# Optimization experiments

Hardware: AMD Instinct MI355X
Metric: run time of the kernel (lower is better)

The kernel has to match this reference:

```python
import jax, jax.numpy as jnp
import numpy as np


def setup_inputs() -> dict:
    key = jax.random.key(0)
    kA, kW = jax.random.split(key, 2)
    T, N = 64, 128  # seq_len, num_peds
    A = jax.random.normal(kA, (T, N, N), dtype=jnp.float32)
    # Linear(2N -> 1): weight stored as (2N, 1), bias (1,)
    W = jax.random.normal(kW, (2 * N, 1), dtype=jnp.float32) * (1.0 / np.sqrt(2 * N))
    b = jnp.zeros((1,), dtype=jnp.float32)
    return {"A": A, "W": W, "b": b}


def reference(A, W, b):
    # A: (T, N, N). Original loops over timesteps; here fully vectorized.
    N = A.shape[2]
    aT = jnp.swapaxes(A, 1, 2)            # a_ = a_.T per timestep -> (T, N, N)
    # Pairwise concat [aT[i], aT[j]] fed to Linear(2N->1) decomposes exactly:
    # score[t,i,j] = aT[t,i]@w1 + aT[t,j]@w2 + b
    w1, w2 = W[:N, 0], W[N:, 0]           # (N,), (N,)
    s1 = aT @ w1                           # (T, N) row-i contribution
    s2 = aT @ w2                           # (T, N) row-j contribution
    e = jax.nn.leaky_relu(s1[:, :, None] + s2[:, None, :] + b[0],
                          negative_slope=0.2)   # (T, N, N)
    alpha = jax.nn.softmax(e, axis=2)      # softmax over neighbor index j (torch dim=1 of (N,N,1))
    # GAT-style aggregation: out[t,i,f] = sum_j alpha[t,i,j] * aT[t,j,f]
    return jnp.einsum('tij,tjf->tif', alpha, aT)
```

## Files before the change

kernel.cpp:

```cpp
#include <hip/hip_runtime.h>

#define NN 128

typedef __attribute__((ext_vector_type(8))) short short8;
typedef __attribute__((ext_vector_type(4))) float f32x4;

__device__ __forceinline__ int SWZ(int r, int cs) {
    return (r << 7) + (cs ^ ((r & 7) << 3));
}

__device__ __forceinline__ unsigned asu(float x) { return __float_as_uint(x); }
__device__ __forceinline__ float asf(unsigned u) { return __uint_as_float(u); }

__global__ __launch_bounds__(256, 2) void gat_fused(
    const float* __restrict__ A, const float* __restrict__ W,
    const float* __restrict__ b, float* __restrict__ out)
{
    __shared__ unsigned short Ah_s[NN * NN];
    __shared__ unsigned short Al_s[NN * NN];
    __shared__ float w_s[2 * NN];
    __shared__ float part1_s[4 * NN], part2_s[4 * NN];
    __shared__ float s1_s[NN], s2_s[NN];

    const int tid  = threadIdx.x;
    const int lane = tid & 63;
    const int wid  = tid >> 6;
    const int t    = blockIdx.x & 63;
    const int i0   = (blockIdx.x >> 6) << 4;
    const float* At = A + (size_t)t * NN * NN;
    const float b0 = b[0];

    if (tid < 64)
        reinterpret_cast<float4*>(w_s)[tid] = reinterpret_cast<const float4*>(W)[tid];
    __syncthreads();

    {
        const float4* A4 = reinterpret_cast<const float4*>(At);
        float p1[4] = {0,0,0,0}, p2[4] = {0,0,0,0};
        #pragma unroll
        for (int it = 0; it < 16; ++it) {
            int e4 = it * 256 + tid;
            int f  = e4 >> 5;
            int cs = (e4 & 31) << 2;
            float4 v = A4[e4];
            float wf1 = w_s[f], wf2 = w_s[NN + f];
            p1[0] += wf1 * v.x; p1[1] += wf1 * v.y; p1[2] += wf1 * v.z; p1[3] += wf1 * v.w;
            p2[0] += wf2 * v.x; p2[1] += wf2 * v.y; p2[2] += wf2 * v.z; p2[3] += wf2 * v.w;
            unsigned ux = asu(v.x), uy = asu(v.y), uz = asu(v.z), uw = asu(v.w);
            float rx = v.x - asf(ux & 0xffff0000u);
            float ry = v.y - asf(uy & 0xffff0000u);
            float rz = v.z - asf(uz & 0xffff0000u);
            float rw = v.w - asf(uw & 0xffff0000u);
            uint2 hv, lv;
            hv.x = (ux >> 16) | (uy & 0xffff0000u);
            hv.y = (uz >> 16) | (uw & 0xffff0000u);
            lv.x = (asu(rx) >> 16) | (asu(ry) & 0xffff0000u);
            lv.y = (asu(rz) >> 16) | (asu(rw) & 0xffff0000u);
            int idx = SWZ(f, cs);
            *reinterpret_cast<uint2*>(&Ah_s[idx]) = hv;
            *reinterpret_cast<uint2*>(&Al_s[idx]) = lv;
        }
        #pragma unroll
        for (int q = 0; q < 4; ++q) {
            p1[q] += __shfl_xor(p1[q], 32);
            p2[q] += __shfl_xor(p2[q], 32);
        }
        if (lane < 32) {
            float4 v1 = { p1[0], p1[1], p1[2], p1[3] };
            float4 v2 = { p2[0], p2[1], p2[2], p2[3] };
            *reinterpret_cast<float4*>(&part1_s[wid * NN + lane * 4]) = v1;
            *reinterpret_cast<float4*>(&part2_s[wid * NN + lane * 4]) = v2;
        }
    }
    __syncthreads();

    if (tid < NN) {
        s1_s[tid] = part1_s[tid] + part1_s[NN + tid]
                  + part1_s[2 * NN + tid] + part1_s[3 * NN + tid] + b0;
        s2_s[tid] = part2_s[tid] + part2_s[NN + tid]
                  + part2_s[2 * NN + tid] + part2_s[3 * NN + tid];
    }
    __syncthreads();

    {
        const int f0 = wid * 32;
        const int ar = lane & 15;
        const int kg = (lane >> 4) << 3;

        short8 bh0[4], bh1[4], bl0[4], bl1[4];
        #pragma unroll
        for (int k = 0; k < 4; ++k) {
            int c = k * 32 + kg;
            bh0[k] = *reinterpret_cast<const short8*>(&Ah_s[SWZ(f0 + ar, c)]);
            bh1[k] = *reinterpret_cast<const short8*>(&Ah_s[SWZ(f0 + 16 + ar, c)]);
            bl0[k] = *reinterpret_cast<const short8*>(&Al_s[SWZ(f0 + ar, c)]);
            bl1[k] = *reinterpret_cast<const short8*>(&Al_s[SWZ(f0 + 16 + ar, c)]);
        }

        float s1v = s1_s[i0 + ar];
        float ev[32];
        float m = -3.4e38f;
        #pragma unroll
        for (int k = 0; k < 4; ++k) {
            float4 sa = *reinterpret_cast<const float4*>(&s2_s[k * 32 + kg]);
            float4 sb = *reinterpret_cast<const float4*>(&s2_s[k * 32 + kg + 4]);
            float xs[8] = { sa.x, sa.y, sa.z, sa.w, sb.x, sb.y, sb.z, sb.w };
            #pragma unroll
            for (int e = 0; e < 8; ++e) {
                float x = s1v + xs[e];
                x = (x >= 0.f) ? x : 0.2f * x;
                ev[k * 8 + e] = x;
                m = fmaxf(m, x);
            }
        }
        m = fmaxf(m, __shfl_xor(m, 16));
        m = fmaxf(m, __shfl_xor(m, 32));
        float s = 0.f;
        #pragma unroll
        for (int c = 0; c < 32; ++c) { ev[c] = __expf(ev[c] - m); s += ev[c]; }
        s += __shfl_xor(s, 16);
        s += __shfl_xor(s, 32);
        float inv = 1.0f / s;

        short8 ah[4], al[4];
        #pragma unroll
        for (int k = 0; k < 4; ++k) {
            union { short8 s8; uint4 u4; } H, L;
            #pragma unroll
            for (int p = 0; p < 4; ++p) {
                float v0 = ev[k * 8 + 2 * p]     * inv;
                float v1 = ev[k * 8 + 2 * p + 1] * inv;
                unsigned u0 = asu(v0), u1 = asu(v1);
                float r0 = v0 - asf(u0 & 0xffff0000u);
                float r1 = v1 - asf(u1 & 0xffff0000u);
                unsigned hw = (u0 >> 16) | (u1 & 0xffff0000u);
                unsigned lw = (asu(r0) >> 16) | (asu(r1) & 0xffff0000u);
                if (p == 0) { H.u4.x = hw; L.u4.x = lw; }
                else if (p == 1) { H.u4.y = hw; L.u4.y = lw; }
                else if (p == 2) { H.u4.z = hw; L.u4.z = lw; }
                else { H.u4.w = hw; L.u4.w = lw; }
            }
            ah[k] = H.s8;
            al[k] = L.s8;
        }

        f32x4 acc0 = {0.f,0.f,0.f,0.f}, acc1 = {0.f,0.f,0.f,0.f};
        #pragma unroll
        for (int k = 0; k < 4; ++k) {
            acc0 = __builtin_amdgcn_mfma_f32_16x16x32_bf16(ah[k], bh0[k], acc0, 0, 0, 0);
            acc1 = __builtin_amdgcn_mfma_f32_16x16x32_bf16(ah[k], bh1[k], acc1, 0, 0, 0);
        }
        #pragma unroll
        for (int k = 0; k < 4; ++k) {
            acc0 = __builtin_amdgcn_mfma_f32_16x16x32_bf16(ah[k], bl0[k], acc0, 0, 0, 0);
            acc1 = __builtin_amdgcn_mfma_f32_16x16x32_bf16(ah[k], bl1[k], acc1, 0, 0, 0);
        }
        #pragma unroll
        for (int k = 0; k < 4; ++k) {
            acc0 = __builtin_amdgcn_mfma_f32_16x16x32_bf16(al[k], bh0[k], acc0, 0, 0, 0);
            acc1 = __builtin_amdgcn_mfma_f32_16x16x32_bf16(al[k], bh1[k], acc1, 0, 0, 0);
        }

        float* outt = out + (size_t)t * NN * NN;
        int orow = i0 + ((lane >> 4) << 2);
        int col  = lane & 15;
        #pragma unroll
        for (int q = 0; q < 4; ++q) {
            outt[(orow + q) * NN + f0 + col]      = acc0[q];
            outt[(orow + q) * NN + f0 + 16 + col] = acc1[q];
        }
    }
}

extern "C" void kernel_launch(void* const* d_in, const int* in_sizes, int n_in,
                              void* d_out, int out_size, void* d_ws, size_t ws_size,
                              hipStream_t stream) {
    const float* A = (const float*)d_in[0];
    const float* W = (const float*)d_in[1];
    const float* b = (const float*)d_in[2];
    float* out = (float*)d_out;
    gat_fused<<<dim3(512), dim3(256), 0, stream>>>(A, W, b, out);
}
```

Measured before the change: 11.64 us.

## Split score computation into separate kernel and drop shared-memory A staging

Replaces the single fused kernel, in which each of 512 blocks recomputed s1/s2 over the whole 128x128 timestep slice and staged it in LDS as bf16 hi/lo, with two kernels. The first computes s1/s2 once per timestep into workspace. The second launches 1024 LDS-free blocks, each loading its own B fragment straight from global memory and splitting it into bf16 hi/lo in registers, with one 16x16 output tile per wave. This removes redundant score computation and the LDS traffic, at the cost of an extra launch, a dependency through global workspace, and B fragments being loaded again by many blocks.

```diff
diff --git a/kernel.cpp b/kernel.cpp
--- a/kernel.cpp
+++ b/kernel.cpp
@@ -5,171 +5,148 @@
 typedef __attribute__((ext_vector_type(8))) short short8;
 typedef __attribute__((ext_vector_type(4))) float f32x4;
 
-__device__ __forceinline__ int SWZ(int r, int cs) {
-    return (r << 7) + (cs ^ ((r & 7) << 3));
-}
-
 __device__ __forceinline__ unsigned asu(float x) { return __float_as_uint(x); }
 __device__ __forceinline__ float asf(unsigned u) { return __uint_as_float(u); }
 
-__global__ __launch_bounds__(256, 2) void gat_fused(
+__device__ __forceinline__ void hilo2(float v0, float v1, unsigned& hw, unsigned& lw) {
+    unsigned u0 = asu(v0), u1 = asu(v1);
+    float r0 = v0 - asf(u0 & 0xffff0000u);
+    float r1 = v1 - asf(u1 & 0xffff0000u);
+    hw = (u0 >> 16) | (u1 & 0xffff0000u);
+    lw = (asu(r0) >> 16) | (asu(r1) & 0xffff0000u);
+}
+
+__global__ __launch_bounds__(256) void s_compute(
     const float* __restrict__ A, const float* __restrict__ W,
-    const float* __restrict__ b, float* __restrict__ out)
+    const float* __restrict__ b, float* __restrict__ s_ws)
 {
-    __shared__ unsigned short Ah_s[NN * NN];
-    __shared__ unsigned short Al_s[NN * NN];
     __shared__ float w_s[2 * NN];
     __shared__ float part1_s[4 * NN], part2_s[4 * NN];
-    __shared__ float s1_s[NN], s2_s[NN];
-
-    const int tid  = threadIdx.x;
-    const int lane = tid & 63;
-    const int wid  = tid >> 6;
-    const int t    = blockIdx.x & 63;
-    const int i0   = (blockIdx.x >> 6) << 4;
+    const int tid = threadIdx.x, lane = tid & 63, wid = tid >> 6;
+    const int t = blockIdx.x;
     const float* At = A + (size_t)t * NN * NN;
-    const float b0 = b[0];
 
     if (tid < 64)
         reinterpret_cast<float4*>(w_s)[tid] = reinterpret_cast<const float4*>(W)[tid];
     __syncthreads();
 
-    {
-        const float4* A4 = reinterpret_cast<const float4*>(At);
-        float p1[4] = {0,0,0,0}, p2[4] = {0,0,0,0};
+    const float4* A4 = reinterpret_cast<const float4*>(At);
+    float p1[4] = {0,0,0,0}, p2[4] = {0,0,0,0};
+    #pragma unroll
+    for (int it = 0; it < 16; ++it) {
+        int e4 = it * 256 + tid;
+        int f  = e4 >> 5;
+        float4 v = A4[e4];
+        float w1 = w_s[f], w2 = w_s[NN + f];
+        p1[0] += w1 * v.x; p1[1] += w1 * v.y; p1[2] += w1 * v.z; p1[3] += w1 * v.w;
+        p2[0] += w2 * v.x; p2[1] += w2 * v.y; p2[2] += w2 * v.z; p2[3] += w2 * v.w;
+    }
+    #pragma unroll
+    for (int q = 0; q < 4; ++q) {
+        p1[q] += __shfl_xor(p1[q], 32);
+        p2[q] += __shfl_xor(p2[q], 32);
+    }
+    if (lane < 32) {
+        float4 v1 = { p1[0], p1[1], p1[2], p1[3] };
+        float4 v2 = { p2[0], p2[1], p2[2], p2[3] };
+        *reinterpret_cast<float4*>(&part1_s[wid * NN + lane * 4]) = v1;
+        *reinterpret_cast<float4*>(&part2_s[wid * NN + lane * 4]) = v2;
+    }
+    __syncthreads();
+    if (tid < NN) {
+        s_ws[t * NN + tid] = part1_s[tid] + part1_s[NN + tid]
+                           + part1_s[2 * NN + tid] + part1_s[3 * NN + tid] + b[0];
+    } else {
+        int c = tid - NN;
+        s_ws[64 * NN + t * NN + c] = part2_s[c] + part2_s[NN + c]
+                                   + part2_s[2 * NN + c] + part2_s[3 * NN + c];
+    }
+}
+
+__global__ __launch_bounds__(256, 4) void gat_pv(
+    const float* __restrict__ A, const float* __restrict__ s_ws,
+    float* __restrict__ out)
+{
+    const int tid  = threadIdx.x;
+    const int lane = tid & 63, wid = tid >> 6;
+    const int bid  = blockIdx.x;
+    const int t    = bid & 63;
+    const int f0   = ((bid >> 6) & 7) << 4;
+    const int i0   = ((bid >> 9) << 6) + (wid << 4);
+    const int r    = lane & 15;
+    const int g    = lane >> 4;
+
+    const float* Brow = A + (size_t)t * NN * NN + (size_t)(f0 + r) * NN + g * 8;
+    float4 bv[8];
+    #pragma unroll
+    for (int k = 0; k < 4; ++k) {
+        bv[2 * k]     = *reinterpret_cast<const float4*>(Brow + 32 * k);
+        bv[2 * k + 1] = *reinterpret_cast<const float4*>(Brow + 32 * k + 4);
+    }
+    const float* s2p = s_ws + 64 * NN + t * NN + g * 8;
+    float4 s2v[8];
+    #pragma unroll
+    for (int k = 0; k < 4; ++k) {
+        s2v[2 * k]     = *reinterpret_cast<const float4*>(s2p + 32 * k);
+        s2v[2 * k + 1] = *reinterpret_cast<const float4*>(s2p + 32 * k + 4);
+    }
+    float s1v = s_ws[t * NN + i0 + r];
+
+    float ev[32];
+    float m = -3.4e38f;
+    #pragma unroll
+    for (int q = 0; q < 8; ++q) {
+        float xs[4] = { s2v[q].x, s2v[q].y, s2v[q].z, s2v[q].w };
         #pragma unroll
-        for (int it = 0; it < 16; ++it) {
-            int e4 = it * 256 + tid;
-            int f  = e4 >> 5;
-            int cs = (e4 & 31) << 2;
-            float4 v = A4[e4];
-            float wf1 = w_s[f], wf2 = w_s[NN + f];
-            p1[0] += wf1 * v.x; p1[1] += wf1 * v.y; p1[2] += wf1 * v.z; p1[3] += wf1 * v.w;
-            p2[0] += wf2 * v.x; p2[1] += wf2 * v.y; p2[2] += wf2 * v.z; p2[3] += wf2 * v.w;
-            unsigned ux = asu(v.x), uy = asu(v.y), uz = asu(v.z), uw = asu(v.w);
-            float rx = v.x - asf(ux & 0xffff0000u);
-            float ry = v.y - asf(uy & 0xffff0000u);
-            float rz = v.z - asf(uz & 0xffff0000u);
-            float rw = v.w - asf(uw & 0xffff0000u);
-            uint2 hv, lv;
-            hv.x = (ux >> 16) | (uy & 0xffff0000u);
-            hv.y = (uz >> 16) | (uw & 0xffff0000u);
-            lv.x = (asu(rx) >> 16) | (asu(ry) & 0xffff0000u);
-            lv.y = (asu(rz) >> 16) | (asu(rw) & 0xffff0000u);
-            int idx = SWZ(f, cs);
-            *reinterpret_cast<uint2*>(&Ah_s[idx]) = hv;
-            *reinterpret_cast<uint2*>(&Al_s[idx]) = lv;
-        }
-        #pragma unroll
-        for (int q = 0; q < 4; ++q) {
-            p1[q] += __shfl_xor(p1[q], 32);
-            p2[q] += __shfl_xor(p2[q], 32);
-        }
-        if (lane < 32) {
-            float4 v1 = { p1[0], p1[1], p1[2], p1[3] };
-            float4 v2 = { p2[0], p2[1], p2[2], p2[3] };
-            *reinterpret_cast<float4*>(&part1_s[wid * NN + lane * 4]) = v1;
-            *reinterpret_cast<float4*>(&part2_s[wid * NN + lane * 4]) = v2;
+        for (int e = 0; e < 4; ++e) {
+            float x = s1v + xs[e];
+            x = (x >= 0.f) ? x : 0.2f * x;
+            ev[q * 4 + e] = x;
+            m = fmaxf(m, x);
         }
     }
-    __syncthreads();
+    m = fmaxf(m, __shfl_xor(m, 16));
+    m = fmaxf(m, __shfl_xor(m, 32));
+    float s = 0.f;
+    #pragma unroll
+    for (int c = 0; c < 32; ++c) { ev[c] = __expf(ev[c] - m); s += ev[c]; }
+    s += __shfl_xor(s, 16);
+    s += __shfl_xor(s, 32);
+    const float inv = 1.0f / s;
 
-    if (tid < NN) {
-        s1_s[tid] = part1_s[tid] + part1_s[NN + tid]
-                  + part1_s[2 * NN + tid] + part1_s[3 * NN + tid] + b0;
-        s2_s[tid] = part2_s[tid] + part2_s[NN + tid]
-                  + part2_s[2 * NN + tid] + part2_s[3 * NN + tid];
+    short8 ah[4], al[4], bh[4], bl[4];
+    #pragma unroll
+    for (int k = 0; k < 4; ++k) {
+        union { short8 s8; unsigned u[4]; } H, L;
+        #pragma unroll
+        for (int p = 0; p < 4; ++p)
+            hilo2(ev[8 * k + 2 * p] * inv, ev[8 * k + 2 * p + 1] * inv, H.u[p], L.u[p]);
+        ah[k] = H.s8; al[k] = L.s8;
     }
-    __syncthreads();
+    #pragma unroll
+    for (int k = 0; k < 4; ++k) {
+        union { short8 s8; unsigned u[4]; } H, L;
+        hilo2(bv[2 * k].x,     bv[2 * k].y,     H.u[0], L.u[0]);
+        hilo2(bv[2 * k].z,     bv[2 * k].w,     H.u[1], L.u[1]);
+        hilo2(bv[2 * k + 1].x, bv[2 * k + 1].y, H.u[2], L.u[2]);
+        hilo2(bv[2 * k + 1].z, bv[2 * k + 1].w, H.u[3], L.u[3]);
+        bh[k] = H.s8; bl[k] = L.s8;
+    }
 
-    {
-        const int f0 = wid * 32;
-        const int ar = lane & 15;
-        const int kg = (lane >> 4) << 3;
+    f32x4 acc = {0.f, 0.f, 0.f, 0.f};
+    #pragma unroll
+    for (int k = 0; k < 4; ++k)
+        acc = __builtin_amdgcn_mfma_f32_16x16x32_bf16(ah[k], bh[k], acc, 0, 0, 0);
+    #pragma unroll
+    for (int k = 0; k < 4; ++k)
+        acc = __builtin_amdgcn_mfma_f32_16x16x32_bf16(ah[k], bl[k], acc, 0, 0, 0);
+    #pragma unroll
+    for (int k = 0; k < 4; ++k)
+        acc = __builtin_amdgcn_mfma_f32_16x16x32_bf16(al[k], bh[k], acc, 0, 0, 0);
 
-        short8 bh0[4], bh1[4], bl0[4], bl1[4];
-        #pragma unroll
-        for (int k = 0; k < 4; ++k) {
-            int c = k * 32 + kg;
-            bh0[k] = *reinterpret_cast<const short8*>(&Ah_s[SWZ(f0 + ar, c)]);
-            bh1[k] = *reinterpret_cast<const short8*>(&Ah_s[SWZ(f0 + 16 + ar, c)]);
-            bl0[k] = *reinterpret_cast<const short8*>(&Al_s[SWZ(f0 + ar, c)]);
-            bl1[k] = *reinterpret_cast<const short8*>(&Al_s[SWZ(f0 + 16 + ar, c)]);
-        }
-
-        float s1v = s1_s[i0 + ar];
-        float ev[32];
-        float m = -3.4e38f;
-        #pragma unroll
-        for (int k = 0; k < 4; ++k) {
-            float4 sa = *reinterpret_cast<const float4*>(&s2_s[k * 32 + kg]);
-            float4 sb = *reinterpret_cast<const float4*>(&s2_s[k * 32 + kg + 4]);
-            float xs[8] = { sa.x, sa.y, sa.z, sa.w, sb.x, sb.y, sb.z, sb.w };
-            #pragma unroll
-            for (int e = 0; e < 8; ++e) {
-                float x = s1v + xs[e];
-                x = (x >= 0.f) ? x : 0.2f * x;
-                ev[k * 8 + e] = x;
-                m = fmaxf(m, x);
-            }
-        }
-        m = fmaxf(m, __shfl_xor(m, 16));
-        m = fmaxf(m, __shfl_xor(m, 32));
-        float s = 0.f;
-        #pragma unroll
-        for (int c = 0; c < 32; ++c) { ev[c] = __expf(ev[c] - m); s += ev[c]; }
-        s += __shfl_xor(s, 16);
-        s += __shfl_xor(s, 32);
-        float inv = 1.0f / s;
-
-        short8 ah[4], al[4];
-        #pragma unroll
-        for (int k = 0; k < 4; ++k) {
-            union { short8 s8; uint4 u4; } H, L;
-            #pragma unroll
-            for (int p = 0; p < 4; ++p) {
-                float v0 = ev[k * 8 + 2 * p]     * inv;
-                float v1 = ev[k * 8 + 2 * p + 1] * inv;
-                unsigned u0 = asu(v0), u1 = asu(v1);
-                float r0 = v0 - asf(u0 & 0xffff0000u);
-                float r1 = v1 - asf(u1 & 0xffff0000u);
-                unsigned hw = (u0 >> 16) | (u1 & 0xffff0000u);
-                unsigned lw = (asu(r0) >> 16) | (asu(r1) & 0xffff0000u);
-                if (p == 0) { H.u4.x = hw; L.u4.x = lw; }
-                else if (p == 1) { H.u4.y = hw; L.u4.y = lw; }
-                else if (p == 2) { H.u4.z = hw; L.u4.z = lw; }
-                else { H.u4.w = hw; L.u4.w = lw; }
-            }
-            ah[k] = H.s8;
-            al[k] = L.s8;
-        }
-
-        f32x4 acc0 = {0.f,0.f,0.f,0.f}, acc1 = {0.f,0.f,0.f,0.f};
-        #pragma unroll
-        for (int k = 0; k < 4; ++k) {
-            acc0 = __builtin_amdgcn_mfma_f32_16x16x32_bf16(ah[k], bh0[k], acc0, 0, 0, 0);
-            acc1 = __builtin_amdgcn_mfma_f32_16x16x32_bf16(ah[k], bh1[k], acc1, 0, 0, 0);
-        }
-        #pragma unroll
-        for (int k = 0; k < 4; ++k) {
-            acc0 = __builtin_amdgcn_mfma_f32_16x16x32_bf16(ah[k], bl0[k], acc0, 0, 0, 0);
-            acc1 = __builtin_amdgcn_mfma_f32_16x16x32_bf16(ah[k], bl1[k], acc1, 0, 0, 0);
-        }
-        #pragma unroll
-        for (int k = 0; k < 4; ++k) {
-            acc0 = __builtin_amdgcn_mfma_f32_16x16x32_bf16(al[k], bh0[k], acc0, 0, 0, 0);
-            acc1 = __builtin_amdgcn_mfma_f32_16x16x32_bf16(al[k], bh1[k], acc1, 0, 0, 0);
-        }
-
-        float* outt = out + (size_t)t * NN * NN;
-        int orow = i0 + ((lane >> 4) << 2);
-        int col  = lane & 15;
-        #pragma unroll
-        for (int q = 0; q < 4; ++q) {
-            outt[(orow + q) * NN + f0 + col]      = acc0[q];
-            outt[(orow + q) * NN + f0 + 16 + col] = acc1[q];
-        }
-    }
+    float* outt = out + (size_t)t * NN * NN + (size_t)(i0 + g * 4) * NN + f0 + r;
+    #pragma unroll
+    for (int q = 0; q < 4; ++q) outt[q * NN] = acc[q];
 }
 
 extern "C" void kernel_launch(void* const* d_in, const int* in_sizes, int n_in,
@@ -178,6 +155,8 @@
     const float* A = (const float*)d_in[0];
     const float* W = (const float*)d_in[1];
     const float* b = (const float*)d_in[2];
-    float* out = (float*)d_out;
-    gat_fused<<<dim3(512), dim3(256), 0, stream>>>(A, W, b, out);
+    float* out  = (float*)d_out;
+    float* s_ws = (float*)d_ws;
+    s_compute<<<dim3(64),   dim3(256), 0, stream>>>(A, W, b, s_ws);
+    gat_pv   <<<dim3(1024), dim3(256), 0, stream>>>(A, s_ws, out);
 }
```

Result: slower. 16.61 us (+42.7%).

## Double block size to 512 threads, one 16-column tile per wave, split MFMA accumulators

Applied to the files above, without the earlier changes.

Raises the block from 256 to 512 threads so the A load/convert loop runs half the iterations per thread, and each of 8 waves now computes a single 16-wide output tile instead of two. The W staging in shared memory and its barrier are removed; weights are read directly from global memory inside the loop. MFMA work is split across two independent accumulators to shorten dependency chains, and the low-part B fragments are loaded later to reduce register pressure. The trade-off is more waves redundantly recomputing softmax per block, and a launch bound of 4 blocks per CU that the ~66KB of shared memory per block cannot actually reach.

```diff
diff --git a/kernel.cpp b/kernel.cpp
--- a/kernel.cpp
+++ b/kernel.cpp
@@ -12,14 +12,14 @@
 __device__ __forceinline__ unsigned asu(float x) { return __float_as_uint(x); }
 __device__ __forceinline__ float asf(unsigned u) { return __uint_as_float(u); }
 
-__global__ __launch_bounds__(256, 2) void gat_fused(
+__global__ __launch_bounds__(512, 4) void gat_fused(
     const float* __restrict__ A, const float* __restrict__ W,
     const float* __restrict__ b, float* __restrict__ out)
 {
     __shared__ unsigned short Ah_s[NN * NN];
     __shared__ unsigned short Al_s[NN * NN];
-    __shared__ float w_s[2 * NN];
-    __shared__ float part1_s[4 * NN], part2_s[4 * NN];
+    __shared__ float part1_s[8 * NN];
+    __shared__ float part2_s[8 * NN];
     __shared__ float s1_s[NN], s2_s[NN];
 
     const int tid  = threadIdx.x;
@@ -28,24 +28,19 @@
     const int t    = blockIdx.x & 63;
     const int i0   = (blockIdx.x >> 6) << 4;
     const float* At = A + (size_t)t * NN * NN;
-    const float b0 = b[0];
-
-    if (tid < 64)
-        reinterpret_cast<float4*>(w_s)[tid] = reinterpret_cast<const float4*>(W)[tid];
-    __syncthreads();
 
     {
         const float4* A4 = reinterpret_cast<const float4*>(At);
         float p1[4] = {0,0,0,0}, p2[4] = {0,0,0,0};
         #pragma unroll
-        for (int it = 0; it < 16; ++it) {
-            int e4 = it * 256 + tid;
+        for (int it = 0; it < 8; ++it) {
+            int e4 = it * 512 + tid;
             int f  = e4 >> 5;
             int cs = (e4 & 31) << 2;
             float4 v = A4[e4];
-            float wf1 = w_s[f], wf2 = w_s[NN + f];
-            p1[0] += wf1 * v.x; p1[1] += wf1 * v.y; p1[2] += wf1 * v.z; p1[3] += wf1 * v.w;
-            p2[0] += wf2 * v.x; p2[1] += wf2 * v.y; p2[2] += wf2 * v.z; p2[3] += wf2 * v.w;
+            float w1 = W[f], w2 = W[NN + f];
+            p1[0] += w1 * v.x; p1[1] += w1 * v.y; p1[2] += w1 * v.z; p1[3] += w1 * v.w;
+            p2[0] += w2 * v.x; p2[1] += w2 * v.y; p2[2] += w2 * v.z; p2[3] += w2 * v.w;
             unsigned ux = asu(v.x), uy = asu(v.y), uz = asu(v.z), uw = asu(v.w);
             float rx = v.x - asf(ux & 0xffff0000u);
             float ry = v.y - asf(uy & 0xffff0000u);
@@ -75,29 +70,31 @@
     __syncthreads();
 
     if (tid < NN) {
-        s1_s[tid] = part1_s[tid] + part1_s[NN + tid]
-                  + part1_s[2 * NN + tid] + part1_s[3 * NN + tid] + b0;
-        s2_s[tid] = part2_s[tid] + part2_s[NN + tid]
-                  + part2_s[2 * NN + tid] + part2_s[3 * NN + tid];
+        float s = b[0];
+        #pragma unroll
+        for (int w = 0; w < 8; ++w) s += part1_s[w * NN + tid];
+        s1_s[tid] = s;
+    } else if (tid < 2 * NN) {
+        int c = tid - NN;
+        float s = 0.f;
+        #pragma unroll
+        for (int w = 0; w < 8; ++w) s += part2_s[w * NN + c];
+        s2_s[c] = s;
     }
     __syncthreads();
 
     {
-        const int f0 = wid * 32;
-        const int ar = lane & 15;
-        const int kg = (lane >> 4) << 3;
+        const int f0 = wid << 4;
+        const int r  = lane & 15;
+        const int g  = lane >> 4;
+        const int kg = g << 3;
 
-        short8 bh0[4], bh1[4], bl0[4], bl1[4];
+        short8 bh[4];
         #pragma unroll
-        for (int k = 0; k < 4; ++k) {
-            int c = k * 32 + kg;
-            bh0[k] = *reinterpret_cast<const short8*>(&Ah_s[SWZ(f0 + ar, c)]);
-            bh1[k] = *reinterpret_cast<const short8*>(&Ah_s[SWZ(f0 + 16 + ar, c)]);
-            bl0[k] = *reinterpret_cast<const short8*>(&Al_s[SWZ(f0 + ar, c)]);
-            bl1[k] = *reinterpret_cast<const short8*>(&Al_s[SWZ(f0 + 16 + ar, c)]);
-        }
+        for (int k = 0; k < 4; ++k)
+            bh[k] = *reinterpret_cast<const short8*>(&Ah_s[SWZ(f0 + r, k * 32 + kg)]);
 
-        float s1v = s1_s[i0 + ar];
+        float s1v = s1_s[i0 + r];
         float ev[32];
         float m = -3.4e38f;
         #pragma unroll
@@ -120,12 +117,12 @@
         for (int c = 0; c < 32; ++c) { ev[c] = __expf(ev[c] - m); s += ev[c]; }
         s += __shfl_xor(s, 16);
         s += __shfl_xor(s, 32);
-        float inv = 1.0f / s;
+        const float inv = 1.0f / s;
 
         short8 ah[4], al[4];
         #pragma unroll
         for (int k = 0; k < 4; ++k) {
-            union { short8 s8; uint4 u4; } H, L;
+            union { short8 s8; unsigned u[4]; } H, L;
             #pragma unroll
             for (int p = 0; p < 4; ++p) {
                 float v0 = ev[k * 8 + 2 * p]     * inv;
@@ -133,42 +130,29 @@
                 unsigned u0 = asu(v0), u1 = asu(v1);
                 float r0 = v0 - asf(u0 & 0xffff0000u);
                 float r1 = v1 - asf(u1 & 0xffff0000u);
-                unsigned hw = (u0 >> 16) | (u1 & 0xffff0000u);
-                unsigned lw = (asu(r0) >> 16) | (asu(r1) & 0xffff0000u);
-                if (p == 0) { H.u4.x = hw; L.u4.x = lw; }
-                else if (p == 1) { H.u4.y = hw; L.u4.y = lw; }
-                else if (p == 2) { H.u4.z = hw; L.u4.z = lw; }
-                else { H.u4.w = hw; L.u4.w = lw; }
+                H.u[p] = (u0 >> 16) | (u1 & 0xffff0000u);
+                L.u[p] = (asu(r0) >> 16) | (asu(r1) & 0xffff0000u);
             }
-            ah[k] = H.s8;
-            al[k] = L.s8;
+            ah[k] = H.s8; al[k] = L.s8;
         }
 
-        f32x4 acc0 = {0.f,0.f,0.f,0.f}, acc1 = {0.f,0.f,0.f,0.f};
+        f32x4 accA = {0.f,0.f,0.f,0.f}, accB = {0.f,0.f,0.f,0.f};
         #pragma unroll
         for (int k = 0; k < 4; ++k) {
-            acc0 = __builtin_amdgcn_mfma_f32_16x16x32_bf16(ah[k], bh0[k], acc0, 0, 0, 0);
-            acc1 = __builtin_amdgcn_mfma_f32_16x16x32_bf16(ah[k], bh1[k], acc1, 0, 0, 0);
+            accA = __builtin_amdgcn_mfma_f32_16x16x32_bf16(ah[k], bh[k], accA, 0, 0, 0);
+            accB = __builtin_amdgcn_mfma_f32_16x16x32_bf16(al[k], bh[k], accB, 0, 0, 0);
         }
+        short8 bl[4];
         #pragma unroll
-        for (int k = 0; k < 4; ++k) {
-            acc0 = __builtin_amdgcn_mfma_f32_16x16x32_bf16(ah[k], bl0[k], acc0, 0, 0, 0);
-            acc1 = __builtin_amdgcn_mfma_f32_16x16x32_bf16(ah[k], bl1[k], acc1, 0, 0, 0);
-        }
+        for (int k = 0; k < 4; ++k)
+            bl[k] = *reinterpret_cast<const short8*>(&Al_s[SWZ(f0 + r, k * 32 + kg)]);
         #pragma unroll
-        for (int k = 0; k < 4; ++k) {
-            acc0 = __builtin_amdgcn_mfma_f32_16x16x32_bf16(al[k], bh0[k], acc0, 0, 0, 0);
-            acc1 = __builtin_amdgcn_mfma_f32_16x16x32_bf16(al[k], bh1[k], acc1, 0, 0, 0);
-        }
+        for (int k = 0; k < 4; ++k)
+            accB = __builtin_amdgcn_mfma_f32_16x16x32_bf16(ah[k], bl[k], accB, 0, 0, 0);
 
-        float* outt = out + (size_t)t * NN * NN;
-        int orow = i0 + ((lane >> 4) << 2);
-        int col  = lane & 15;
+        float* outt = out + (size_t)t * NN * NN + (size_t)(i0 + g * 4) * NN + f0 + r;
         #pragma unroll
-        for (int q = 0; q < 4; ++q) {
-            outt[(orow + q) * NN + f0 + col]      = acc0[q];
-            outt[(orow + q) * NN + f0 + 16 + col] = acc1[q];
-        }
+        for (int q = 0; q < 4; ++q) outt[q * NN] = accA[q] + accB[q];
     }
 }
 
@@ -179,5 +163,5 @@
     const float* W = (const float*)d_in[1];
     const float* b = (const float*)d_in[2];
     float* out = (float*)d_out;
-    gat_fused<<<dim3(512), dim3(256), 0, stream>>>(A, W, b, out);
+    gat_fused<<<dim3(512), dim3(512), 0, stream>>>(A, W, b, out);
 }
```

New measurement: 12.48 us. +7.2%, slower.
